# Kernel optimization log

Hardware: AMD Instinct MI355X
Metric: run time of the kernel (lower is better)

The kernel has to match this reference:

```python
import jax, jax.numpy as jnp
import numpy as np

B, D, N, H = 2, 512, 2048, 8
DK = D // H
EPS = 1e-5


def conv1x1(x, w, b):
    # kernel-size-1 Conv1d == channel-mixing GEMM: (o,i) x (b,i,n) -> (b,o,n)
    return jnp.einsum('oi,bin->bon', w, x) + b[None, :, None]


def setup_inputs() -> dict:
    key = jax.random.key(0)
    ks = jax.random.split(key, 20)
    s = 0.02
    return {
        'init_query': jax.random.normal(ks[0], (B, D, N), jnp.float32),
        'key_t': jax.random.normal(ks[1], (B, D, N), jnp.float32),
        'value': jax.random.normal(ks[2], (B, D, N), jnp.float32),
        'mask': jax.random.randint(ks[3], (B, 1, N, N), 0, 2, jnp.int32),
        'Wq': jax.random.normal(ks[4], (D, D), jnp.float32) * s,
        'bq': jax.random.normal(ks[5], (D,), jnp.float32) * s,
        'Wk': jax.random.normal(ks[6], (D, D), jnp.float32) * s,
        'bk': jax.random.normal(ks[7], (D,), jnp.float32) * s,
        'Wv': jax.random.normal(ks[8], (D, D), jnp.float32) * s,
        'bv': jax.random.normal(ks[9], (D,), jnp.float32) * s,
        'Wm': jax.random.normal(ks[10], (D, D), jnp.float32) * s,
        'bm': jax.random.normal(ks[11], (D,), jnp.float32) * s,
        'W1': jax.random.normal(ks[12], (2 * D, 2 * D), jnp.float32) * s,
        'b1': jax.random.normal(ks[13], (2 * D,), jnp.float32) * s,
        'gamma': jnp.ones((2 * D,), jnp.float32),
        'beta': jnp.zeros((2 * D,), jnp.float32),
        'rmean': jax.random.normal(ks[14], (2 * D,), jnp.float32) * s,
        'rvar': jnp.abs(jax.random.normal(ks[15], (2 * D,), jnp.float32)) * 0.1 + 0.5,
        'W2': jax.random.normal(ks[16], (D, 2 * D), jnp.float32) * s,
        'b2': jnp.zeros((D,), jnp.float32),  # nn.init.constant_(bias, 0.0)
    }


def reference(init_query, key_t, value, mask, Wq, bq, Wk, bk, Wv, bv, Wm, bm,
              W1, b1, gamma, beta, rmean, rvar, W2, b2):
    # projections, split channels into (d_k, n_heads) exactly like torch .view
    q = conv1x1(init_query, Wq, bq).reshape(B, DK, H, N)
    k = conv1x1(key_t, Wk, bk).reshape(B, DK, H, N)
    v = conv1x1(value, Wv, bv).reshape(B, DK, H, N)
    scores = jnp.einsum('bdhn,bdhm->bhnm', q, k) / jnp.sqrt(jnp.float32(DK))
    scores = jnp.where(mask == 0, jnp.float32(-1e9), scores)
    attn = jax.nn.softmax(scores, axis=-1)
    x = jnp.einsum('bhnm,bdhm->bdhn', attn, v).reshape(B, D, N)
    x = conv1x1(x, Wm, bm)
    x = jnp.concatenate([x, init_query], axis=1)  # (B, 2D, N)
    h = conv1x1(x, W1, b1)
    # BatchNorm1d (inference mode with running stats) + ReLU
    h = (h - rmean[None, :, None]) * (gamma / jnp.sqrt(rvar + EPS))[None, :, None] + beta[None, :, None]
    h = jax.nn.relu(h)
    return conv1x1(h, W2, b2)
```

## Files before the change

### kernel.cpp

```cpp
#include <hip/hip_runtime.h>

typedef unsigned short u16;
typedef unsigned int u32;
typedef unsigned long long u64;
typedef long long i64;
typedef __bf16 bf16x8 __attribute__((ext_vector_type(8)));
typedef u16 u16x8 __attribute__((ext_vector_type(8)));
typedef float f32x4 __attribute__((ext_vector_type(4)));
typedef float f32x16 __attribute__((ext_vector_type(16)));

#define DEV __device__ __forceinline__

constexpr int BB = 2, DD = 512, NN = 2048, HH = 8, DKc = 64, D2 = 1024;

constexpr float QSC = 0.125f * 1.44269504088896340736f;

constexpr i64 MB = 1048576;
constexpr i64 OFF_CAT = 0;
constexpr i64 OFF_XKT = 8 * MB;
constexpr i64 OFF_XVT = 12 * MB;
constexpr i64 OFF_QH  = 16 * MB;
constexpr i64 OFF_KH  = 20 * MB;
constexpr i64 OFF_VT  = 24 * MB;
constexpr i64 OFF_HT  = 28 * MB;
constexpr i64 OFF_OP  = 36 * MB;
constexpr i64 OFF_LP  = 68 * MB;
constexpr i64 OFF_WQP = 69 * MB;
constexpr i64 OFF_WKP = 69 * MB + 524288;
constexpr i64 OFF_WVP = 69 * MB + 1048576;
constexpr i64 OFF_WMT = 69 * MB + 1572864;
constexpr i64 OFF_W1A = 71 * MB;
constexpr i64 OFF_W1C = 72 * MB;
constexpr i64 OFF_W2B = 74 * MB;
constexpr i64 OFF_BQP = 75 * MB;
constexpr i64 OFF_BKP = 75 * MB + 2048;
constexpr i64 OFF_BVP = 75 * MB + 4096;
constexpr i64 OFF_BNA = 75 * MB + 8192;
constexpr i64 OFF_BNC = 75 * MB + 12288;
constexpr i64 OFF_MSK = 76 * MB;

DEV u16 f2bf(float f) {
  u32 u = __float_as_uint(f);
  u = u + 0x7FFFu + ((u >> 16) & 1u);
  return (u16)(u >> 16);
}

DEV float bf2f(u16 u) { return __uint_as_float(((u32)u) << 16); }

DEV u32 packbf(float lo, float hi) {
  return __builtin_amdgcn_perm(__float_as_uint(hi), __float_as_uint(lo), 0x07060302u);
}

DEV float fexp2(float x) {
#if __has_builtin(__builtin_amdgcn_exp2f)
  return __builtin_amdgcn_exp2f(x);
#else
  return exp2f(x);
#endif
}

DEV bf16x8 ldfrag(const u16* p) {
  bf16x8 v;
  __builtin_memcpy(&v, __builtin_assume_aligned(p, 16), 16);
  return v;
}

DEV bf16x8 ldfrag8(const u16* p) {
  bf16x8 v;
  __builtin_memcpy(&v, __builtin_assume_aligned(p, 8), 16);
  return v;
}

DEV bf16x8 ones8() {
  u16x8 u = {0x3F80, 0x3F80, 0x3F80, 0x3F80, 0x3F80, 0x3F80, 0x3F80, 0x3F80};
  bf16x8 v;
  __builtin_memcpy(&v, &u, 16);
  return v;
}

DEV void gload16(const void* g, void* lds) {
  __builtin_amdgcn_global_load_lds((__attribute__((address_space(1))) void*)g,
                                   (__attribute__((address_space(3))) void*)lds, 16, 0, 0);
}

DEV f32x4 mfma16(bf16x8 a, bf16x8 b, f32x4 c) {
  return __builtin_amdgcn_mfma_f32_16x16x32_bf16(a, b, c, 0, 0, 0);
}

DEV f32x16 mfma32(bf16x8 a, bf16x8 b, f32x16 c) {
  return __builtin_amdgcn_mfma_f32_32x32x16_bf16(a, b, c, 0, 0, 0);
}

__global__ __launch_bounds__(256) void prep_all(
    const float* __restrict__ Wq, const float* __restrict__ Wk, const float* __restrict__ Wv,
    const float* __restrict__ Wm, const float* __restrict__ W1, const float* __restrict__ W2,
    const float* __restrict__ bq, const float* __restrict__ bk, const float* __restrict__ bv,
    const float* __restrict__ bm, const float* __restrict__ b1, const float* __restrict__ gamma_,
    const float* __restrict__ beta_, const float* __restrict__ rmean,
    const float* __restrict__ rvar, const int* __restrict__ mask,
    const float* __restrict__ iq, const float* __restrict__ kt, const float* __restrict__ vv,
    u16* __restrict__ wqp, u16* __restrict__ wkp, u16* __restrict__ wvp, u16* __restrict__ wmt,
    u16* __restrict__ w1a, u16* __restrict__ w1c, u16* __restrict__ w2b,
    float* __restrict__ bqp, float* __restrict__ bkp, float* __restrict__ bvp,
    float* __restrict__ bna, float* __restrict__ bnc, u32* __restrict__ mw,
    u16* __restrict__ cat, u16* __restrict__ xkt, u16* __restrict__ xvt) {
  __shared__ float tile[32][33];
  const int blk = blockIdx.x, t = threadIdx.x;
  if (blk < 768) {
    const int which = blk >> 8, lb = blk & 255;
    const float* W = which == 0 ? Wq : (which == 1 ? Wk : Wv);
    u16* dst = which == 0 ? wqp : (which == 1 ? wkp : wvp);
    for (int e = lb * 256 + t; e < 262144; e += 65536) {
      int op = e >> 9, i = e & 511;
      int dk = op & 63, h = op >> 6;
      dst[e] = f2bf(W[(dk * 8 + h) * 512 + i]);
    }
  } else if (blk < 1024) {
    const int lb = blk - 768;
    for (int e = lb * 256 + t; e < 262144; e += 65536) {
      int cp = e >> 9, o = e & 511;
      int dk = cp & 63, h = cp >> 6;
      wmt[e] = f2bf(Wm[o * 512 + dk * 8 + h]);
    }
  } else if (blk < 1280) {
    const int lb = blk - 1024;
    for (int e = lb * 256 + t; e < 524288; e += 65536) {
      int row = e >> 9, o = e & 511;
      w1a[e] = f2bf(W1[(i64)row * 1024 + o]);
    }
  } else if (blk < 1536) {
    const int lb = blk - 1280;
    for (int e = lb * 256 + t; e < 524288; e += 65536) {
      int row = e >> 9, j = e & 511;
      w1c[(i64)row * 1024 + 512 + j] = f2bf(W1[(i64)row * 1024 + 512 + j]);
    }
  } else if (blk < 1792) {
    const int lb = blk - 1536;
    for (int e = lb * 256 + t; e < 524288; e += 65536) w2b[e] = f2bf(W2[e]);
  } else if (blk < 1808) {
    __shared__ float sm[4][64];
    const int base = (blk - 1792) * 64;
    const int el = t & 63, oq = t >> 6;
    const float* wrow = W1 + (i64)(base + el) * 1024 + oq * 128;
    const float* bmq = bm + oq * 128;
    float s = 0.f;
#pragma unroll 8
    for (int j = 0; j < 128; j += 4) {
      float4 x = *(const float4*)(wrow + j);
      float4 y = *(const float4*)(bmq + j);
      s += x.x * y.x + x.y * y.y + x.z * y.z + x.w * y.w;
    }
    sm[oq][el] = s;
    __syncthreads();
    if (t < 64) {
      int e = base + t;
      float a = gamma_[e] * rsqrtf(rvar[e] + 1e-5f);
      bna[e] = a;
      bnc[e] = (b1[e] - rmean[e]) * a + beta_[e] + a * (sm[0][t] + sm[1][t] + sm[2][t] + sm[3][t]);
    }
  } else if (blk == 1808) {
    for (int e = t; e < 512; e += 256) {
      int src = (e & 63) * 8 + (e >> 6);
      bqp[e] = bq[src]; bkp[e] = bk[src]; bvp[e] = bv[src];
    }
  } else if (blk < 2833) {
    const int tid = (blk - 1809) * 256 + t;
    const int l = tid & 63, mt = (tid >> 6) & 31, g = (tid >> 11) & 63, b = tid >> 17;
    const int kv0 = mt * 64 + (l & 31);
    u32 word = 0;
#pragma unroll
    for (int reg = 0; reg < 16; ++reg) {
      int r = (reg & 3) + 8 * (reg >> 2) + 4 * (l >> 5);
      const int* mp = mask + ((i64)b * NN + g * 32 + r) * NN + kv0;
      word |= (mp[0] != 0 ? (1u << (2 * reg)) : 0u) | (mp[32] != 0 ? (2u << (2 * reg)) : 0u);
    }
    mw[tid] = word;
  } else {
    const int idx = blk - 2833;
    const int bx = idx & 63, by = (idx >> 6) & 15, bz = idx >> 10;
    const int tensor = bz >> 1, b = bz & 1;
    const float* src = (tensor == 0 ? iq : (tensor == 1 ? kt : vv)) + (i64)b * DD * NN;
    u16* dst; i64 ldd; int coff;
    if (tensor == 0)      { dst = cat + (i64)b * NN * D2; ldd = D2; coff = DD; }
    else if (tensor == 1) { dst = xkt + (i64)b * NN * DD; ldd = DD; coff = 0; }
    else                  { dst = xvt + (i64)b * NN * DD; ldd = DD; coff = 0; }
    const int x0 = bx * 32, y0 = by * 32;
    const int col = t & 31, rg = t >> 5;
#pragma unroll
    for (int i = 0; i < 4; ++i) {
      int row = rg + i * 8;
      tile[row][col] = src[(i64)(y0 + row) * NN + x0 + col];
    }
    __syncthreads();
    const int dp = t & 15, rbase = t >> 4;
    u32* dst32 = (u32*)dst;
    const i64 ldw = ldd >> 1;
    const int cw = (coff + y0) >> 1;
#pragma unroll
    for (int i = 0; i < 2; ++i) {
      int rr = rbase + i * 16;
      dst32[(i64)(x0 + rr) * ldw + cw + dp] = packbf(tile[2 * dp][rr], tile[2 * dp + 1][rr]);
    }
  }
}

template <int AM, int AN>
DEV void gemm_core(const u16* __restrict__ A, i64 lda, const u16* __restrict__ Bp, i64 ldb,
                   int K, u16* As, u16* Bs, f32x4 (&acc)[AM][AN]) {
  constexpr int BM = AM * 32, BN = AN * 32;
  const int t = threadIdx.x, w = t >> 6, l = t & 63, quad = l >> 4, l15 = l & 15;
  const int wm = (w >> 1) * AM * 16, wn = (w & 1) * AN * 16;
  for (int kk = 0; kk < K; kk += 64) {
    __syncthreads();
#pragma unroll
    for (int j = 0; j < BM / 32; ++j) {
      int ch = j * 256 + w * 64 + l, r = ch >> 3, c = ch & 7;
      gload16(A + (i64)r * lda + kk + ((c ^ (r & 7)) << 3), As + (j * 256 + w * 64) * 8);
    }
#pragma unroll
    for (int j = 0; j < BN / 32; ++j) {
      int ch = j * 256 + w * 64 + l, r = ch >> 3, c = ch & 7;
      gload16(Bp + (i64)r * ldb + kk + ((c ^ (r & 7)) << 3), Bs + (j * 256 + w * 64) * 8);
    }
    __syncthreads();
#pragma unroll
    for (int kc = 0; kc < 2; ++kc) {
      const int sw = ((kc * 4 + quad) ^ (l15 & 7)) << 3;
      bf16x8 af[AM], bfr[AN];
#pragma unroll
      for (int i = 0; i < AM; ++i) af[i] = ldfrag(&As[(wm + i * 16 + l15) * 64 + sw]);
#pragma unroll
      for (int j = 0; j < AN; ++j) bfr[j] = ldfrag(&Bs[(wn + j * 16 + l15) * 64 + sw]);
#pragma unroll
      for (int i = 0; i < AM; ++i)
#pragma unroll
        for (int j = 0; j < AN; ++j) acc[i][j] = mfma16(af[i], bfr[j], acc[i][j]);
    }
  }
}

__global__ __launch_bounds__(256) void qkv_gemm(const u16* __restrict__ cat,
                                                const u16* __restrict__ xkt,
                                                const u16* __restrict__ xvt,
                                                const u16* __restrict__ wqp,
                                                const u16* __restrict__ wkp,
                                                const u16* __restrict__ wvp,
                                                const u16* __restrict__ w1a,
                                                const u16* __restrict__ wmt,
                                                const float* __restrict__ bqp,
                                                const float* __restrict__ bkp,
                                                const float* __restrict__ bvp,
                                                u16* __restrict__ qh, u16* __restrict__ kh,
                                                u16* __restrict__ vt, u16* __restrict__ w1c) {
  __shared__ __align__(16) u16 As[128 * 64];
  __shared__ __align__(16) u16 Bs[64 * 64];
  const int z = blockIdx.z, b = z & 1;
  const int op = (z == 6) ? 3 : (z >> 1);
  const int t = threadIdx.x, w = t >> 6, l = t & 63, quad = l >> 4, l15 = l & 15;
  const int wm = (w >> 1) * 64, wn = (w & 1) * 32;
  int mx, ny;
  const u16 *A, *Bp;
  i64 lda, ldb;
  if (op < 2) {
    mx = blockIdx.x; ny = blockIdx.y;
    A = (op == 0 ? cat + DD : xkt);
    lda = (op == 0 ? D2 : DD);
    A += (i64)b * NN * lda + (i64)mx * 128 * lda;
    Bp = (op == 0 ? wqp : wkp) + (i64)ny * 64 * DD;
    ldb = DD;
  } else if (op == 2) {
    int f = blockIdx.x * 8 + blockIdx.y;
    mx = f >> 5; ny = f & 31;
    A = wvp + (i64)mx * 128 * DD; lda = DD;
    Bp = xvt + (i64)b * NN * DD + (i64)ny * 64 * DD; ldb = DD;
  } else {
    if (blockIdx.x >= 8) return;
    mx = blockIdx.x; ny = blockIdx.y;
    A = w1a + (i64)mx * 128 * DD; lda = DD;
    Bp = wmt + (i64)ny * 64 * DD; ldb = DD;
  }
  f32x4 acc[4][2] = {};
  gemm_core<4, 2>(A, lda, Bp, ldb, DD, As, Bs, acc);

  const int rowBase = mx * 128 + wm + quad * 4;
  const int colBase = ny * 64 + wn + l15;
  if (op < 2) {
    const float* bias = (op == 0 ? bqp : bkp);
    const float sc = (op == 0 ? QSC : 1.f);
    u16* dst = (op == 0 ? qh : kh) + (i64)b * HH * NN * DKc;
#pragma unroll
    for (int j = 0; j < 2; ++j) {
      const int col = colBase + j * 16;
      const float cA = bias[col];
#pragma unroll
      for (int i = 0; i < 4; ++i)
#pragma unroll
        for (int r = 0; r < 4; ++r) {
          const int row = rowBase + i * 16 + r;
          dst[(i64)(col >> 6) * (NN * 64) + (i64)row * 64 + (col & 63)] =
              f2bf((acc[i][j][r] + cA) * sc);
        }
    }
  } else if (op == 2) {
    u16* dst = vt + (i64)b * HH * DKc * NN;
#pragma unroll
    for (int j = 0; j < 2; ++j) {
      const int col = colBase + j * 16;
      const int colp = (col & ~63) | (((col & 31) << 1) | ((col >> 5) & 1));
#pragma unroll
      for (int i = 0; i < 4; ++i)
#pragma unroll
        for (int r = 0; r < 4; ++r) {
          const int row = rowBase + i * 16 + r;
          dst[(i64)row * NN + colp] = f2bf(acc[i][j][r] + bvp[row]);
        }
    }
  } else {
#pragma unroll
    for (int j = 0; j < 2; ++j) {
      const int col = colBase + j * 16;
#pragma unroll
      for (int i = 0; i < 4; ++i)
#pragma unroll
        for (int r = 0; r < 4; ++r) {
          const int row = rowBase + i * 16 + r;
          w1c[(i64)row * D2 + col] = f2bf(acc[i][j][r]);
        }
    }
  }
}

struct GArgs {
  const u16* A; i64 lda, sAb;
  const u16* B; i64 ldb, sBb;
  void* C; i64 ldc, sCb;
  const float* p1; const float* p2;
  int K;
};

template <int MODE, int AM, int AN>
__global__ __launch_bounds__(256) void gemm_bt(GArgs g) {
  __shared__ __align__(16) u16 As[AM * 32 * 64];
  __shared__ __align__(16) u16 Bs[AN * 32 * 64];
  const int t = threadIdx.x, w = t >> 6, l = t & 63, quad = l >> 4, l15 = l & 15;
  const int wm = (w >> 1) * AM * 16, wn = (w & 1) * AN * 16;
  const int bz = blockIdx.z;
  const u16* A = g.A + (i64)bz * g.sAb + (i64)blockIdx.x * (AM * 32) * g.lda;
  const u16* Bp = g.B + (i64)bz * g.sBb + (i64)blockIdx.y * (AN * 32) * g.ldb;
  f32x4 acc[AM][AN] = {};
  gemm_core<AM, AN>(A, g.lda, Bp, g.ldb, g.K, As, Bs, acc);

  const int rowBase = blockIdx.x * (AM * 32) + wm + quad * 4;
  const int colBase = blockIdx.y * (AN * 32) + wn + l15;
#pragma unroll
  for (int j = 0; j < AN; ++j) {
    const int col = colBase + j * 16;
    float cA = 0.f, cB = 0.f;
    if (MODE == 3) { cA = g.p1[col]; cB = g.p2[col]; }
#pragma unroll
    for (int i = 0; i < AM; ++i) {
#pragma unroll
      for (int r = 0; r < 4; ++r) {
        const int row = rowBase + i * 16 + r;
        float v = acc[i][j][r];
        if (MODE == 3) {
          float x = v * cA + cB;
          ((u16*)g.C + (i64)bz * g.sCb)[(i64)row * g.ldc + col] = f2bf(x > 0.f ? x : 0.f);
        } else {
          ((float*)g.C + (i64)bz * g.sCb)[(i64)row * g.ldc + col] = v + g.p1[row];
        }
      }
    }
  }
}

__global__ __launch_bounds__(256) void flash_attn(const u16* __restrict__ Qh,
                                                  const u16* __restrict__ Kh,
                                                  const u16* __restrict__ Vt,
                                                  const u32* __restrict__ MW2,
                                                  u16* __restrict__ Opart,
                                                  float* __restrict__ Lp) {
  __shared__ __align__(16) u16 Ks[64 * 64];
  __shared__ __align__(16) u16 Vs[64 * 64];
  __shared__ __align__(16) u16 Ps[4][32 * 68];
  const int t = threadIdx.x, w = t >> 6, l = t & 63, l31 = l & 31, lh = l >> 5;
  const int nt = blockIdx.x, h = blockIdx.y, b = blockIdx.z >> 2, sp = blockIdx.z & 3;
  const u16* Qb = Qh + ((i64)(b * HH + h) * NN + nt * 128 + w * 32) * 64;
  const u16* Kb = Kh + (i64)(b * HH + h) * NN * 64;
  const u16* Vb = Vt + (i64)(b * HH + h) * 64 * NN;
  const u32* MWb = MW2 + ((i64)(b * 64 + nt * 4 + w) * 32) * 64 + l;
  const bf16x8 ONE = ones8();
  bf16x8 qf[4];
#pragma unroll
  for (int kc = 0; kc < 4; ++kc)
    __builtin_memcpy(&qf[kc], Qb + (i64)l31 * 64 + kc * 16 + lh * 8, 16);

  f32x16 oacc0 = {}, oacc1 = {}, lacc = {};
  for (int mt = sp * 8; mt < sp * 8 + 8; ++mt) {
    __syncthreads();
#pragma unroll
    for (int j = 0; j < 2; ++j) {
      int ch = j * 256 + t, r = ch >> 3, c = ch & 7;
      gload16(Kb + (i64)(mt * 64 + r) * 64 + ((c ^ (r & 7)) << 3), &Ks[ch * 8]);
      gload16(Vb + (i64)r * NN + mt * 64 + ((c ^ (r & 7)) << 3), &Vs[ch * 8]);
    }
    __syncthreads();
    f32x16 s0 = {}, s1 = {};
#pragma unroll
    for (int kc = 0; kc < 4; ++kc) {
      const int r1 = 32 + l31;
      bf16x8 k0 = ldfrag(&Ks[l31 * 64 + (((kc * 2 + lh) ^ (l31 & 7)) << 3)]);
      bf16x8 k1 = ldfrag(&Ks[r1 * 64 + (((kc * 2 + lh) ^ (r1 & 7)) << 3)]);
      s0 = mfma32(qf[kc], k0, s0);
      s1 = mfma32(qf[kc], k1, s1);
    }
    const u32 mword = MWb[(i64)mt * 64];
#pragma unroll
    for (int reg = 0; reg < 16; ++reg) {
      const int row = (reg & 3) + 8 * (reg >> 2) + 4 * lh;
      u32 sh = mword >> (2 * reg);
      u32 m01 = ((sh & 1u) | ((sh & 2u) << 15)) * 0xFFFFu;
      u32 pv = packbf(fexp2(s0[reg]), fexp2(s1[reg])) & m01;
      *(u32*)__builtin_assume_aligned(&Ps[w][row * 68 + l31 * 2], 4) = pv;
    }
    asm volatile("" ::: "memory");
    bf16x8 pf[4];
#pragma unroll
    for (int kc = 0; kc < 4; ++kc) pf[kc] = ldfrag8(&Ps[w][l31 * 68 + kc * 16 + lh * 8]);
#pragma unroll
    for (int kc = 0; kc < 4; ++kc) lacc = mfma32(pf[kc], ONE, lacc);
#pragma unroll
    for (int kc = 0; kc < 4; ++kc) {
      const int r1 = 32 + l31;
      bf16x8 v0 = ldfrag(&Vs[l31 * 64 + (((kc * 2 + lh) ^ (l31 & 7)) << 3)]);
      bf16x8 v1 = ldfrag(&Vs[r1 * 64 + (((kc * 2 + lh) ^ (r1 & 7)) << 3)]);
      oacc0 = mfma32(pf[kc], v0, oacc0);
      oacc1 = mfma32(pf[kc], v1, oacc1);
    }
  }
  u16* Op = Opart + (i64)sp * (BB * NN * DD) + ((i64)b * NN + nt * 128 + w * 32) * DD + h * 64;
#pragma unroll
  for (int reg = 0; reg < 16; ++reg) {
    const int row = (reg & 3) + 8 * (reg >> 2) + 4 * lh;
    Op[(i64)row * DD + l31] = f2bf(oacc0[reg]);
    Op[(i64)row * DD + 32 + l31] = f2bf(oacc1[reg]);
  }
  if (l31 == 0) {
    float* Lpb = Lp + ((i64)(sp * BB + b) * HH + h) * NN + nt * 128 + w * 32;
#pragma unroll
    for (int reg = 0; reg < 16; ++reg)
      Lpb[(reg & 3) + 8 * (reg >> 2) + 4 * lh] = lacc[reg];
  }
}

__global__ __launch_bounds__(256) void combine(const u16* __restrict__ Opart,
                                               const float* __restrict__ Lp,
                                               u16* __restrict__ cat) {
  const int tid = blockIdx.x * 256 + threadIdx.x;
  const int b = tid >> 18, rem = tid & 262143;
  const int n = rem >> 7, cq = rem & 127;
  const int c0 = cq << 2, h = c0 >> 6;
  const i64 base = ((i64)b * NN + n) * DD + c0;
  const i64 stride = (i64)BB * NN * DD;
  float acc[4] = {0.f, 0.f, 0.f, 0.f};
  float lsum = 0.f;
#pragma unroll
  for (int s = 0; s < 4; ++s) {
    u16 a[4];
    __builtin_memcpy(a, __builtin_assume_aligned(Opart + s * stride + base, 8), 8);
#pragma unroll
    for (int j = 0; j < 4; ++j) acc[j] += bf2f(a[j]);
    lsum += Lp[((i64)(s * BB + b) * HH + h) * NN + n];
  }
  float rl = __builtin_amdgcn_rcpf(lsum);
  u16 o[4];
#pragma unroll
  for (int j = 0; j < 4; ++j) o[j] = f2bf(acc[j] * rl);
  __builtin_memcpy(__builtin_assume_aligned(&cat[((i64)b * NN + n) * D2 + c0], 8), o, 8);
}

extern "C" void kernel_launch(void* const* d_in, const int* in_sizes, int n_in,
                              void* d_out, int out_size, void* d_ws, size_t ws_size,
                              hipStream_t stream) {
  (void)in_sizes; (void)n_in; (void)out_size; (void)ws_size;
  const float* iq    = (const float*)d_in[0];
  const float* kt    = (const float*)d_in[1];
  const float* vv    = (const float*)d_in[2];
  const int*   mask  = (const int*)d_in[3];
  const float* Wq    = (const float*)d_in[4];
  const float* bq    = (const float*)d_in[5];
  const float* Wk    = (const float*)d_in[6];
  const float* bk    = (const float*)d_in[7];
  const float* Wv    = (const float*)d_in[8];
  const float* bv    = (const float*)d_in[9];
  const float* Wm    = (const float*)d_in[10];
  const float* bm    = (const float*)d_in[11];
  const float* W1    = (const float*)d_in[12];
  const float* b1    = (const float*)d_in[13];
  const float* gamma_= (const float*)d_in[14];
  const float* beta_ = (const float*)d_in[15];
  const float* rmean = (const float*)d_in[16];
  const float* rvar  = (const float*)d_in[17];
  const float* W2    = (const float*)d_in[18];
  const float* b2    = (const float*)d_in[19];

  char* ws = (char*)d_ws;
  u16* cat = (u16*)(ws + OFF_CAT);
  u16* xkt = (u16*)(ws + OFF_XKT);
  u16* xvt = (u16*)(ws + OFF_XVT);
  u16* qh  = (u16*)(ws + OFF_QH);
  u16* kh  = (u16*)(ws + OFF_KH);
  u16* vt  = (u16*)(ws + OFF_VT);
  u16* ht  = (u16*)(ws + OFF_HT);
  u16* opart = (u16*)(ws + OFF_OP);
  float* lp  = (float*)(ws + OFF_LP);
  u16* wqp = (u16*)(ws + OFF_WQP);
  u16* wkp = (u16*)(ws + OFF_WKP);
  u16* wvp = (u16*)(ws + OFF_WVP);
  u16* wmt = (u16*)(ws + OFF_WMT);
  u16* w1a = (u16*)(ws + OFF_W1A);
  u16* w1c = (u16*)(ws + OFF_W1C);
  u16* w2b = (u16*)(ws + OFF_W2B);
  float* bqp = (float*)(ws + OFF_BQP);
  float* bkp = (float*)(ws + OFF_BKP);
  float* bvp = (float*)(ws + OFF_BVP);
  float* bna = (float*)(ws + OFF_BNA);
  float* bnc = (float*)(ws + OFF_BNC);
  u32* mw = (u32*)(ws + OFF_MSK);

  prep_all<<<8977, 256, 0, stream>>>(Wq, Wk, Wv, Wm, W1, W2, bq, bk, bv, bm, b1, gamma_, beta_,
                                     rmean, rvar, mask, iq, kt, vv, wqp, wkp, wvp, wmt, w1a, w1c,
                                     w2b, bqp, bkp, bvp, bna, bnc, mw, cat, xkt, xvt);
  qkv_gemm<<<dim3(16, 8, 7), 256, 0, stream>>>(cat, xkt, xvt, wqp, wkp, wvp, w1a, wmt,
                                               bqp, bkp, bvp, qh, kh, vt, w1c);
  flash_attn<<<dim3(16, 8, 8), 256, 0, stream>>>(qh, kh, vt, mw, opart, lp);
  combine<<<2048, 256, 0, stream>>>(opart, lp, cat);
  GArgs wa{cat, D2, (i64)NN * D2, w1c, D2, 0, ht, D2, (i64)NN * D2, bna, bnc, D2};
  gemm_bt<3, 2, 2><<<dim3(32, 16, 2), 256, 0, stream>>>(wa);
  GArgs w2a{w2b, D2, 0, ht, D2, (i64)NN * D2, d_out, NN, (i64)DD * NN, b2, nullptr, D2};
  gemm_bt<4, 2, 2><<<dim3(8, 32, 2), 256, 0, stream>>>(w2a);
}
```

Measured before the change: 219.0 us.

## Remap block indices for L2 locality, widen combine, retile first FFN GEMM

Flash attention now uses a flat 1D grid with heads varying fastest, so blocks sharing the same mask rows run at the same time. The W2 GEMM gets a block swizzle that groups tiles sharing weight rows to improve cache reuse. The combine kernel moves to 8-element (16-byte) vectors with half as many threads. The W1 GEMM treats both batches as one M=4096 problem with a 4x2 tile (128-row blocks), which gives fewer, larger blocks and may lower occupancy.

```diff
diff --git a/kernel.cpp b/kernel.cpp
--- a/kernel.cpp
+++ b/kernel.cpp
@@ -338,20 +338,28 @@
   int K;
 };
 
-template <int MODE, int AM, int AN>
+template <int MODE, int AM, int AN, int SWZ>
 __global__ __launch_bounds__(256) void gemm_bt(GArgs g) {
   __shared__ __align__(16) u16 As[AM * 32 * 64];
   __shared__ __align__(16) u16 Bs[AN * 32 * 64];
   const int t = threadIdx.x, w = t >> 6, l = t & 63, quad = l >> 4, l15 = l & 15;
   const int wm = (w >> 1) * AM * 16, wn = (w & 1) * AN * 16;
-  const int bz = blockIdx.z;
-  const u16* A = g.A + (i64)bz * g.sAb + (i64)blockIdx.x * (AM * 32) * g.lda;
-  const u16* Bp = g.B + (i64)bz * g.sBb + (i64)blockIdx.y * (AN * 32) * g.ldb;
+  int bx = blockIdx.x, by = blockIdx.y, bz = blockIdx.z;
+  if (SWZ == 1) {
+    const int i = bx + (by << 3) + (bz << 8);
+    const int slot = i & 7, jj = i >> 3;
+    by = slot + ((jj & 3) << 3);
+    const int j2 = jj >> 2;
+    bx = j2 & 7;
+    bz = j2 >> 3;
+  }
+  const u16* A = g.A + (i64)bz * g.sAb + (i64)bx * (AM * 32) * g.lda;
+  const u16* Bp = g.B + (i64)bz * g.sBb + (i64)by * (AN * 32) * g.ldb;
   f32x4 acc[AM][AN] = {};
   gemm_core<AM, AN>(A, g.lda, Bp, g.ldb, g.K, As, Bs, acc);
 
-  const int rowBase = blockIdx.x * (AM * 32) + wm + quad * 4;
-  const int colBase = blockIdx.y * (AN * 32) + wn + l15;
+  const int rowBase = bx * (AM * 32) + wm + quad * 4;
+  const int colBase = by * (AN * 32) + wn + l15;
 #pragma unroll
   for (int j = 0; j < AN; ++j) {
     const int col = colBase + j * 16;
@@ -384,7 +392,11 @@
   __shared__ __align__(16) u16 Vs[64 * 64];
   __shared__ __align__(16) u16 Ps[4][32 * 68];
   const int t = threadIdx.x, w = t >> 6, l = t & 63, l31 = l & 31, lh = l >> 5;
-  const int nt = blockIdx.x, h = blockIdx.y, b = blockIdx.z >> 2, sp = blockIdx.z & 3;
+  const int flat = blockIdx.x;
+  const int h = flat & 7;
+  const int j = flat >> 3;
+  const int nt = j & 15, zz = j >> 4;
+  const int b = zz >> 2, sp = zz & 3;
   const u16* Qb = Qh + ((i64)(b * HH + h) * NN + nt * 128 + w * 32) * 64;
   const u16* Kb = Kh + (i64)(b * HH + h) * NN * 64;
   const u16* Vb = Vt + (i64)(b * HH + h) * 64 * NN;
@@ -399,8 +411,8 @@
   for (int mt = sp * 8; mt < sp * 8 + 8; ++mt) {
     __syncthreads();
 #pragma unroll
-    for (int j = 0; j < 2; ++j) {
-      int ch = j * 256 + t, r = ch >> 3, c = ch & 7;
+    for (int j2 = 0; j2 < 2; ++j2) {
+      int ch = j2 * 256 + t, r = ch >> 3, c = ch & 7;
       gload16(Kb + (i64)(mt * 64 + r) * 64 + ((c ^ (r & 7)) << 3), &Ks[ch * 8]);
       gload16(Vb + (i64)r * NN + mt * 64 + ((c ^ (r & 7)) << 3), &Vs[ch * 8]);
     }
@@ -457,26 +469,26 @@
                                                const float* __restrict__ Lp,
                                                u16* __restrict__ cat) {
   const int tid = blockIdx.x * 256 + threadIdx.x;
-  const int b = tid >> 18, rem = tid & 262143;
-  const int n = rem >> 7, cq = rem & 127;
-  const int c0 = cq << 2, h = c0 >> 6;
+  const int b = tid >> 17, rem = tid & 131071;
+  const int n = rem >> 6, cg = rem & 63;
+  const int c0 = cg << 3, h = cg >> 3;
   const i64 base = ((i64)b * NN + n) * DD + c0;
   const i64 stride = (i64)BB * NN * DD;
-  float acc[4] = {0.f, 0.f, 0.f, 0.f};
+  float acc[8] = {};
   float lsum = 0.f;
 #pragma unroll
   for (int s = 0; s < 4; ++s) {
-    u16 a[4];
-    __builtin_memcpy(a, __builtin_assume_aligned(Opart + s * stride + base, 8), 8);
-#pragma unroll
-    for (int j = 0; j < 4; ++j) acc[j] += bf2f(a[j]);
+    u16 a[8];
+    __builtin_memcpy(a, __builtin_assume_aligned(Opart + s * stride + base, 16), 16);
+#pragma unroll
+    for (int j = 0; j < 8; ++j) acc[j] += bf2f(a[j]);
     lsum += Lp[((i64)(s * BB + b) * HH + h) * NN + n];
   }
   float rl = __builtin_amdgcn_rcpf(lsum);
-  u16 o[4];
-#pragma unroll
-  for (int j = 0; j < 4; ++j) o[j] = f2bf(acc[j] * rl);
-  __builtin_memcpy(__builtin_assume_aligned(&cat[((i64)b * NN + n) * D2 + c0], 8), o, 8);
+  u16 o[8];
+#pragma unroll
+  for (int j = 0; j < 8; ++j) o[j] = f2bf(acc[j] * rl);
+  __builtin_memcpy(__builtin_assume_aligned(&cat[((i64)b * NN + n) * D2 + c0], 16), o, 16);
 }
 
 extern "C" void kernel_launch(void* const* d_in, const int* in_sizes, int n_in,
@@ -533,10 +545,10 @@
                                      w2b, bqp, bkp, bvp, bna, bnc, mw, cat, xkt, xvt);
   qkv_gemm<<<dim3(16, 8, 7), 256, 0, stream>>>(cat, xkt, xvt, wqp, wkp, wvp, w1a, wmt,
                                                bqp, bkp, bvp, qh, kh, vt, w1c);
-  flash_attn<<<dim3(16, 8, 8), 256, 0, stream>>>(qh, kh, vt, mw, opart, lp);
-  combine<<<2048, 256, 0, stream>>>(opart, lp, cat);
-  GArgs wa{cat, D2, (i64)NN * D2, w1c, D2, 0, ht, D2, (i64)NN * D2, bna, bnc, D2};
-  gemm_bt<3, 2, 2><<<dim3(32, 16, 2), 256, 0, stream>>>(wa);
+  flash_attn<<<1024, 256, 0, stream>>>(qh, kh, vt, mw, opart, lp);
+  combine<<<1024, 256, 0, stream>>>(opart, lp, cat);
+  GArgs wa{cat, D2, 0, w1c, D2, 0, ht, D2, 0, bna, bnc, D2};
+  gemm_bt<3, 4, 2, 0><<<dim3(32, 16, 1), 256, 0, stream>>>(wa);
   GArgs w2a{w2b, D2, 0, ht, D2, (i64)NN * D2, d_out, NN, (i64)DD * NN, b2, nullptr, D2};
-  gemm_bt<4, 2, 2><<<dim3(8, 32, 2), 256, 0, stream>>>(w2a);
-}
+  gemm_bt<4, 2, 2, 1><<<dim3(8, 32, 2), 256, 0, stream>>>(w2a);
+}
```

After: 222.3 us. About the same (+1.5%).
